# Performance work log

Measured on AMD Instinct MI355X. Metric: run time of the kernel, lower is better.

## Reference

```python
import jax, jax.numpy as jnp
import numpy as np

NUM_USERS = 10000
NUM_POIS = 50000
SEQ_LEN = 100
EMB = 128
HEADS = 8
NUM_NODES = NUM_USERS + NUM_POIS + 1  # +1 padding node (last row)
N_LOCAL = 2
N_GLOBAL = 2
B = 1024
NNZ_G = 1920000
NNZ_H = 1600000


def spmm(rows, cols, vals, x, n):
    # torch.sparse.mm(COO, x): gather rows of x by cols, scale, scatter-add by rows
    return jax.ops.segment_sum(vals[:, None] * x[cols], rows, num_segments=n)


def mha(x, in_w, in_b, out_w, out_b):
    # torch.nn.MultiheadAttention (batch_first, eval mode, self-attention)
    b, l, d = x.shape
    hd = d // HEADS
    qkv = x @ in_w.T + in_b  # [b, l, 3d]
    q, k, v = jnp.split(qkv, 3, axis=-1)
    def split_heads(t):
        return t.reshape(b, l, HEADS, hd).transpose(0, 2, 1, 3)  # [b,h,l,hd]
    q, k, v = split_heads(q), split_heads(k), split_heads(v)
    scores = jnp.einsum('bhqd,bhkd->bhqk', q, k) / jnp.sqrt(jnp.asarray(hd, x.dtype))
    attn = jax.nn.softmax(scores, axis=-1)
    o = jnp.einsum('bhqk,bhkd->bhqd', attn, v)
    o = o.transpose(0, 2, 1, 3).reshape(b, l, d)
    return o @ out_w.T + out_b


def setup_inputs():
    key = jax.random.key(0)
    ks = jax.random.split(key, 32)
    stdv = 1.0 / np.sqrt(EMB)
    def u(k, shape):
        return jax.random.uniform(k, shape, jnp.float32, -stdv, stdv)
    inp = {}
    # --- learned parameters ---
    inp['nodes_emb'] = u(ks[0], (NUM_NODES, EMB)).at[NUM_NODES - 1].set(0.0)  # padding_idx
    inp['pos_emb_local'] = u(ks[1], (SEQ_LEN + 1, EMB)).at[0].set(0.0)
    inp['fc_geo_w'] = u(ks[2], (EMB, EMB))
    inp['fc_geo_b'] = u(ks[3], (EMB,))
    inp['in_proj_w'] = u(ks[4], (3 * EMB, EMB))
    inp['in_proj_b'] = u(ks[5], (3 * EMB,))
    inp['out_proj_w'] = u(ks[6], (EMB, EMB))
    inp['out_proj_b'] = u(ks[7], (EMB,))
    inp['pos_emb_glob'] = u(ks[8], (SEQ_LEN + 1, EMB)).at[0].set(0.0)
    inp['w1_w'] = u(ks[9], (EMB, 2 * EMB))
    inp['w1_b'] = u(ks[10], (EMB,))
    inp['w_2'] = u(ks[11], (EMB, 1))
    inp['glu1_w'] = u(ks[12], (EMB, EMB))
    inp['glu1_b'] = u(ks[13], (EMB,))
    inp['glu2_w'] = u(ks[14], (EMB, EMB))
    # --- sparse graphs (COO) ---
    inp['G_rows'] = jax.random.randint(ks[15], (NNZ_G,), 0, NUM_NODES - 1, jnp.int32)
    inp['G_cols'] = jax.random.randint(ks[16], (NNZ_G,), 0, NUM_NODES - 1, jnp.int32)
    inp['G_vals'] = jax.random.uniform(ks[17], (NNZ_G,), jnp.float32) * (1.0 / 32.0)
    inp['HG_rows'] = jax.random.randint(ks[18], (NNZ_H,), 0, NUM_POIS, jnp.int32)
    inp['HG_cols'] = jax.random.randint(ks[19], (NNZ_H,), 0, NUM_POIS, jnp.int32)
    inp['HG_vals'] = jax.random.uniform(ks[20], (NNZ_H,), jnp.float32) * (1.0 / 32.0)
    # --- batch tensors ---
    inp['batch_users_seqs'] = jax.random.randint(ks[21], (B, SEQ_LEN), 0, NUM_NODES - 1, jnp.int32)
    inp['batch_users_seqs_masks'] = jax.random.randint(ks[22], (B, SEQ_LEN), 0, 2, jnp.int32)
    inp['batch_users_geo_adjs'] = jax.random.uniform(ks[23], (B, SEQ_LEN, SEQ_LEN), jnp.float32) * (1.0 / SEQ_LEN)
    inp['batch_users_indices'] = jnp.arange(B, dtype=jnp.int32)
    inp['batch_seqs_lens'] = 1.0 + jax.random.uniform(ks[24], (B,), jnp.float32) * (SEQ_LEN - 1)
    inp['batch_users_rev_seqs'] = jax.random.randint(ks[25], (B, SEQ_LEN), 0, NUM_NODES - 1, jnp.int32)
    return inp


def reference(nodes_emb, pos_emb_local, fc_geo_w, fc_geo_b, in_proj_w, in_proj_b,
              out_proj_w, out_proj_b, pos_emb_glob, w1_w, w1_b, w_2, glu1_w, glu1_b,
              glu2_w, G_rows, G_cols, G_vals, HG_rows, HG_cols, HG_vals,
              batch_users_seqs, batch_users_seqs_masks, batch_users_geo_adjs,
              batch_users_indices, batch_seqs_lens, batch_users_rev_seqs):
    pos_local = pos_emb_local[jnp.arange(1, SEQ_LEN + 1)]  # [L, D], same for all batches

    def st_layer(nodes):
        seq_e = nodes[batch_users_seqs]  # [B, L, D] gather
        geo_e = jnp.einsum('bls,bsd->bld', batch_users_geo_adjs, seq_e)
        geo_e = jax.nn.relu(geo_e @ fc_geo_w.T + fc_geo_b)
        tot = seq_e + pos_local[None] + geo_e
        o = mha(tot, in_proj_w, in_proj_b, out_proj_w, out_proj_b)
        users = jnp.mean(o, axis=1)  # [B, D]
        nodes = nodes.at[batch_users_indices].set(users)  # scatter
        core = spmm(G_rows, G_cols, G_vals, nodes[:-1], NUM_NODES - 1)
        return nodes.at[:-1].set(core)

    # local spatial-temporal graph: shared layer applied N_LOCAL times, layer-mean
    nodes = nodes_emb
    acc = nodes
    for _ in range(N_LOCAL):
        nodes = st_layer(nodes)
        acc = acc + nodes
    local = acc / (N_LOCAL + 1)

    local_users = local[batch_users_indices]
    local_pois = local[NUM_USERS:-1]

    # global hypergraph convolution on POI embeddings, layer-mean
    x = nodes_emb[NUM_USERS:-1]
    acc_g = x
    for _ in range(N_GLOBAL):
        x = spmm(HG_rows, HG_cols, HG_vals, x, NUM_POIS)
        acc_g = acc_g + x
    global_pois = acc_g / (N_GLOBAL + 1)

    pois_embs = local_pois + global_pois
    fusion = jnp.concatenate([local[:NUM_USERS], pois_embs,
                              jnp.zeros((1, EMB), local.dtype)], axis=0)

    # user temporal preference augmentation
    seq_h = fusion[batch_users_rev_seqs]  # [B, L, D]
    hs = jnp.sum(seq_h, axis=1) / batch_seqs_lens[:, None]  # [B, D]
    pos_idx = jnp.arange(1, SEQ_LEN + 1, dtype=jnp.int32)[None] * batch_users_seqs_masks
    pos_e = pos_emb_glob[pos_idx]  # [B, L, D]; masked positions hit padding row 0
    nh = jnp.tanh(jnp.concatenate([pos_e, seq_h], axis=-1) @ w1_w.T + w1_b)
    nh = jax.nn.sigmoid(nh @ glu1_w.T + glu1_b + hs[:, None, :] @ glu2_w.T)
    beta = nh @ w_2  # [B, L, 1]
    select = jnp.sum(beta * seq_h, axis=1)  # [B, D]

    batch_users_embs = select + local_users
    return batch_users_embs, pois_embs
```

## Files before the change

### kernel.cpp

```cpp
#include <hip/hip_runtime.h>
#include <hip/hip_bf16.h>
#include <math.h>

typedef __hip_bfloat16 bf16;

__device__ __forceinline__ float b2f(bf16 x){ return __bfloat162float(x); }
__device__ __forceinline__ bf16  f2b(float x){ return __float2bfloat16(x); }

__device__ __forceinline__ short f2bs(float f){
    unsigned u = __float_as_uint(f);
    u += 0x7fffu + ((u >> 16) & 1u);
    return (short)(u >> 16);
}
__device__ __forceinline__ float bs2f(short s){
    return __uint_as_float(((unsigned)(unsigned short)s) << 16);
}

#define NUSERS   10000
#define NPOIS    50000
#define SEQL     100
#define NNODES   60001
#define BATCH    1024
#define NNZG     1920000
#define NNZH     1600000
#define BL       (BATCH*SEQL)
#define BLD      (BL*128)
#define NND      (NNODES*128)
#define CN       (60000*128)
#define PD       (NPOIS*128)

__device__ __forceinline__ void  stc(bf16* p,  float v){ *p = f2b(v); }
__device__ __forceinline__ void  stc(float* p, float v){ *p = v; }

typedef __attribute__((ext_vector_type(8))) short s16x8;
typedef __attribute__((ext_vector_type(4))) float f32x4;

__global__ __launch_bounds__(256) void k_zero(float* __restrict__ p, int n4){
    int i = blockIdx.x*256 + threadIdx.x;
    if (i < n4) ((float4*)p)[i] = make_float4(0.f,0.f,0.f,0.f);
}

__global__ __launch_bounds__(256) void k_copy16(ulong2* __restrict__ dst,
                                                const ulong2* __restrict__ src, int n16){
    int i = blockIdx.x*256 + threadIdx.x;
    if (i < n16) dst[i] = src[i];
}

__global__ __launch_bounds__(256) void k_init(bf16* __restrict__ nodes, float* __restrict__ acc,
                                              const float* __restrict__ src, int n){
    int i = blockIdx.x*256 + threadIdx.x;
    if (i >= n) return;
    float v = src[i];
    nodes[i] = f2b(v); acc[i] = v;
}

__global__ __launch_bounds__(256) void k_gather_f(float* __restrict__ dst,
                                                  const float* __restrict__ table,
                                                  const int* __restrict__ idx, int rows){
    int gid = blockIdx.x*256 + threadIdx.x;
    if (gid >= rows*128) return;
    int r = gid >> 7, c = gid & 127;
    dst[(size_t)r*128 + c] = table[(size_t)idx[r]*128 + c];
}

__global__ __launch_bounds__(256) void k_mgeo2(bf16* __restrict__ tot,
                                               const bf16* __restrict__ nodes,
                                               const int* __restrict__ seqs,
                                               const float* __restrict__ adj,
                                               const float* __restrict__ fcw,
                                               const float* __restrict__ fcb,
                                               const float* __restrict__ posl){
    __shared__ short st[128*104];
    __shared__ short gt[112*136];
    int b = blockIdx.x, tid = threadIdx.x;
    const int* sq = seqs + b*SEQL;
    for (int i = tid; i < SEQL*128; i += 256){
        int j = i >> 7, c = i & 127;
        st[c*104 + j] = ((const short*)nodes)[(size_t)sq[j]*128 + c];
    }
    for (int i = tid; i < 128*4; i += 256){ int c = i>>2, r = i&3; st[c*104 + 100 + r] = 0; }
    __syncthreads();
    int wv = tid>>6, lane = tid&63, lr = lane&15, lk = lane>>4;
    const s16x8 zf = {0,0,0,0,0,0,0,0};
    s16x8 bfr[2][4];
    #pragma unroll
    for (int t = 0; t < 2; t++){
        int nt = wv*2 + t;
        #pragma unroll
        for (int kc = 0; kc < 4; kc++)
            bfr[t][kc] = *(const s16x8*)&st[(nt*16+lr)*104 + kc*32 + lk*8];
    }
    const float* ab = adj + (size_t)b*SEQL*SEQL;
    for (int mt = 0; mt < 7; mt++){
        int ar = min(mt*16 + lr, SEQL-1);
        s16x8 ah[4], al[4];
        #pragma unroll
        for (int kc = 0; kc < 4; kc++){
            float av[8] = {0,0,0,0,0,0,0,0};
            if (kc < 3){
                const float* ap = ab + (size_t)ar*SEQL + kc*32 + lk*8;
                float4 a0 = *(const float4*)ap;
                float4 a1 = *(const float4*)(ap + 4);
                av[0]=a0.x; av[1]=a0.y; av[2]=a0.z; av[3]=a0.w;
                av[4]=a1.x; av[5]=a1.y; av[6]=a1.z; av[7]=a1.w;
            } else if (lk == 0){
                float4 a0 = *(const float4*)(ab + (size_t)ar*SEQL + 96);
                av[0]=a0.x; av[1]=a0.y; av[2]=a0.z; av[3]=a0.w;
            }
            s16x8 h = zf, l = zf;
            #pragma unroll
            for (int j = 0; j < 8; j++){
                short hb = f2bs(av[j]);
                h[j] = hb;
                l[j] = f2bs(av[j] - bs2f(hb));
            }
            ah[kc] = h; al[kc] = l;
        }
        f32x4 c0 = {0.f,0.f,0.f,0.f}, c1 = {0.f,0.f,0.f,0.f};
        #pragma unroll
        for (int kc = 0; kc < 4; kc++){
            c0 = __builtin_amdgcn_mfma_f32_16x16x32_bf16(ah[kc], bfr[0][kc], c0, 0,0,0);
            c0 = __builtin_amdgcn_mfma_f32_16x16x32_bf16(al[kc], bfr[0][kc], c0, 0,0,0);
            c1 = __builtin_amdgcn_mfma_f32_16x16x32_bf16(ah[kc], bfr[1][kc], c1, 0,0,0);
            c1 = __builtin_amdgcn_mfma_f32_16x16x32_bf16(al[kc], bfr[1][kc], c1, 0,0,0);
        }
        #pragma unroll
        for (int t = 0; t < 2; t++){
            f32x4 cc = t ? c1 : c0;
            int col = wv*32 + t*16 + lr;
            #pragma unroll
            for (int r = 0; r < 4; r++){
                int row = mt*16 + lk*4 + r;
                gt[row*136 + col] = f2bs(cc[r]);
            }
        }
    }
    s16x8 wh[2][4], wl[2][4];
    int n0 = wv*32;
    #pragma unroll
    for (int t = 0; t < 2; t++){
        #pragma unroll
        for (int ks = 0; ks < 4; ks++){
            const float* wp = fcw + (size_t)(n0 + t*16 + lr)*128 + ks*32 + lk*8;
            float4 w0 = *(const float4*)(wp);
            float4 w1 = *(const float4*)(wp + 4);
            float wf[8] = {w0.x,w0.y,w0.z,w0.w,w1.x,w1.y,w1.z,w1.w};
            s16x8 h, l;
            #pragma unroll
            for (int j = 0; j < 8; j++){
                short hb = f2bs(wf[j]);
                h[j] = hb;
                l[j] = f2bs(wf[j] - bs2f(hb));
            }
            wh[t][ks] = h; wl[t][ks] = l;
        }
    }
    __syncthreads();
    for (int mt = 0; mt < 7; mt++){
        s16x8 ah[4];
        #pragma unroll
        for (int ks = 0; ks < 4; ks++)
            ah[ks] = *(const s16x8*)&gt[(mt*16+lr)*136 + ks*32 + lk*8];
        f32x4 c0 = {0.f,0.f,0.f,0.f}, c1 = {0.f,0.f,0.f,0.f};
        #pragma unroll
        for (int ks = 0; ks < 4; ks++){
            c0 = __builtin_amdgcn_mfma_f32_16x16x32_bf16(ah[ks], wh[0][ks], c0, 0,0,0);
            c0 = __builtin_amdgcn_mfma_f32_16x16x32_bf16(ah[ks], wl[0][ks], c0, 0,0,0);
            c1 = __builtin_amdgcn_mfma_f32_16x16x32_bf16(ah[ks], wh[1][ks], c1, 0,0,0);
            c1 = __builtin_amdgcn_mfma_f32_16x16x32_bf16(ah[ks], wl[1][ks], c1, 0,0,0);
        }
        #pragma unroll
        for (int t = 0; t < 2; t++){
            f32x4 cc = t ? c1 : c0;
            int col = n0 + t*16 + lr;
            float bv = fcb[col];
            #pragma unroll
            for (int r = 0; r < 4; r++){
                int row = mt*16 + lk*4 + r;
                if (row < SEQL){
                    float v = fmaxf(cc[r] + bv, 0.f);
                    v += bs2f(st[col*104 + row]) + posl[(row+1)*128 + col];
                    tot[(size_t)b*SEQL*128 + (size_t)row*128 + col] = f2b(v);
                }
            }
        }
    }
}

template<typename TA, typename TC>
__global__ __launch_bounds__(256) void k_mgemm(const TA* __restrict__ A,
                                               const float* __restrict__ W, int wstride, int woff,
                                               const float* __restrict__ bias, int boff,
                                               TC* __restrict__ C, int act,
                                               const float* __restrict__ add1, int addmode,
                                               const int* __restrict__ masks){
    constexpr bool A_BF = (sizeof(TA) == 2);
    int tid  = threadIdx.x;
    int wv   = tid >> 6;
    int lane = tid & 63;
    int lr   = lane & 15;
    int lk   = lane >> 4;
    int n0   = wv * 32;

    s16x8 wh[2][4], wl[2][4];
    #pragma unroll
    for (int t = 0; t < 2; t++){
        #pragma unroll
        for (int ks = 0; ks < 4; ks++){
            const float* wp = W + (size_t)(n0 + t*16 + lr)*wstride + woff + ks*32 + lk*8;
            float4 w0 = *(const float4*)(wp);
            float4 w1 = *(const float4*)(wp + 4);
            float wf[8] = {w0.x,w0.y,w0.z,w0.w,w1.x,w1.y,w1.z,w1.w};
            s16x8 h, l;
            #pragma unroll
            for (int j = 0; j < 8; j++){
                short hb = f2bs(wf[j]);
                h[j] = hb;
                l[j] = f2bs(wf[j] - bs2f(hb));
            }
            wh[t][ks] = h; wl[t][ks] = l;
        }
    }

    size_t mblk = (size_t)blockIdx.x * 128;
    for (int it = 0; it < 8; it++){
        size_t m0 = mblk + (size_t)it*16;
        s16x8 ah[4], al[4];
        #pragma unroll
        for (int ks = 0; ks < 4; ks++){
            if constexpr (A_BF){
                ah[ks] = *(const s16x8*)((const short*)A + (m0 + lr)*128 + ks*32 + lk*8);
            } else {
                const float* ap = (const float*)A + (m0 + lr)*128 + ks*32 + lk*8;
                float4 a0 = *(const float4*)(ap);
                float4 a1 = *(const float4*)(ap + 4);
                float av[8] = {a0.x,a0.y,a0.z,a0.w,a1.x,a1.y,a1.z,a1.w};
                s16x8 h, l;
                #pragma unroll
                for (int j = 0; j < 8; j++){
                    short hb = f2bs(av[j]);
                    h[j] = hb;
                    l[j] = f2bs(av[j] - bs2f(hb));
                }
                ah[ks] = h; al[ks] = l;
            }
        }
        __syncthreads();
        f32x4 c0 = {0.f,0.f,0.f,0.f}, c1 = {0.f,0.f,0.f,0.f};
        #pragma unroll
        for (int ks = 0; ks < 4; ks++){
            c0 = __builtin_amdgcn_mfma_f32_16x16x32_bf16(ah[ks], wh[0][ks], c0, 0, 0, 0);
            c0 = __builtin_amdgcn_mfma_f32_16x16x32_bf16(ah[ks], wl[0][ks], c0, 0, 0, 0);
            c1 = __builtin_amdgcn_mfma_f32_16x16x32_bf16(ah[ks], wh[1][ks], c1, 0, 0, 0);
            c1 = __builtin_amdgcn_mfma_f32_16x16x32_bf16(ah[ks], wl[1][ks], c1, 0, 0, 0);
            if constexpr (!A_BF){
                c0 = __builtin_amdgcn_mfma_f32_16x16x32_bf16(al[ks], wh[0][ks], c0, 0, 0, 0);
                c1 = __builtin_amdgcn_mfma_f32_16x16x32_bf16(al[ks], wh[1][ks], c1, 0, 0, 0);
            }
        }
        #pragma unroll
        for (int t = 0; t < 2; t++){
            f32x4 cc = t ? c1 : c0;
            int c = n0 + t*16 + lr;
            float bv = bias ? bias[boff + c] : 0.f;
            #pragma unroll
            for (int r4 = 0; r4 < 4; r4++){
                int m = (int)m0 + lk*4 + r4;
                float v = cc[r4] + bv;
                if (addmode == 1){
                    int l = m % SEQL;
                    int p = (l+1) * masks[m];
                    v += add1[p*128 + c];
                } else if (addmode == 2){
                    v += add1[(m/SEQL)*128 + c];
                }
                if (act == 1) v = fmaxf(v, 0.f);
                else if (act == 2) v = tanhf(v);
                else if (act == 3) v = 1.f/(1.f+__expf(-v));
                stc(&C[(size_t)m*128 + c], v);
            }
        }
    }
}

__global__ __launch_bounds__(256) void k_mattn(bf16* o, const bf16* Qq,
                                               const bf16* Qk, const bf16* Qv){
    __shared__ short Vt[128*104];
    __shared__ short Ph[4][16*136];
    __shared__ short Pl[4][16*136];
    int b = blockIdx.x, tid = threadIdx.x;
    const short* vsrc = (const short*)(Qv + (size_t)b*SEQL*128);
    for (int i = tid; i < SEQL*128; i += 256){ int j = i>>7, c = i&127; Vt[c*104 + j] = vsrc[i]; }
    for (int i = tid; i < 128*4; i += 256){ int c = i>>2, r = i&3; Vt[c*104 + 100 + r] = 0; }
    int wv = tid>>6, lane = tid&63, lr = lane&15, lk = lane>>4;
    short* phw = Ph[wv];
    short* plw = Pl[wv];
    for (int i = lane; i < 16*136; i += 64){ phw[i] = 0; plw[i] = 0; }
    __syncthreads();

    const s16x8 zf = {0,0,0,0,0,0,0,0};
    size_t rowbase = (size_t)b*SEQL*128;
    bool kreal = (lk < 2);
    for (int hh = 0; hh < 2; hh++){
        int h = wv*2 + hh;
        int hd = h*16 + lk*8;
        s16x8 kf[7];
        #pragma unroll
        for (int nt = 0; nt < 7; nt++){
            int kr = min(nt*16 + lr, SEQL-1);
            kf[nt] = kreal ? *(const s16x8*)((const short*)Qk + rowbase + (size_t)kr*128 + hd) : zf;
        }
        s16x8 vf[4];
        #pragma unroll
        for (int kc = 0; kc < 4; kc++)
            vf[kc] = *(const s16x8*)&Vt[(h*16+lr)*104 + kc*32 + lk*8];

        for (int mt = 0; mt < 7; mt++){
            int qr = min(mt*16 + lr, SEQL-1);
            s16x8 qf = kreal ? *(const s16x8*)((const short*)Qq + rowbase + (size_t)qr*128 + hd) : zf;
            f32x4 sc[7];
            #pragma unroll
            for (int nt = 0; nt < 7; nt++){
                f32x4 z = {0.f,0.f,0.f,0.f};
                sc[nt] = __builtin_amdgcn_mfma_f32_16x16x32_bf16(qf, kf[nt], z, 0,0,0);
            }
            float mx[4] = {-1e30f,-1e30f,-1e30f,-1e30f};
            #pragma unroll
            for (int nt = 0; nt < 7; nt++){
                bool masked = (nt == 6) && (lr >= 4);
                #pragma unroll
                for (int r = 0; r < 4; r++){
                    float s = masked ? -1e30f : sc[nt][r]*0.25f;
                    sc[nt][r] = s;
                    mx[r] = fmaxf(mx[r], s);
                }
            }
            #pragma unroll
            for (int m = 1; m < 16; m <<= 1){
                #pragma unroll
                for (int r = 0; r < 4; r++) mx[r] = fmaxf(mx[r], __shfl_xor(mx[r], m));
            }
            float sm[4] = {0.f,0.f,0.f,0.f};
            #pragma unroll
            for (int nt = 0; nt < 7; nt++){
                #pragma unroll
                for (int r = 0; r < 4; r++){
                    float p = __expf(sc[nt][r] - mx[r]);
                    sc[nt][r] = p; sm[r] += p;
                }
            }
            #pragma unroll
            for (int m = 1; m < 16; m <<= 1){
                #pragma unroll
                for (int r = 0; r < 4; r++) sm[r] += __shfl_xor(sm[r], m);
            }
            float inv[4];
            #pragma unroll
            for (int r = 0; r < 4; r++) inv[r] = 1.f/sm[r];
            #pragma unroll
            for (int nt = 0; nt < 7; nt++){
                #pragma unroll
                for (int r = 0; r < 4; r++){
                    float p = sc[nt][r]*inv[r];
                    short hb = f2bs(p);
                    int pa = (lk*4+r)*136 + nt*16 + lr;
                    phw[pa] = hb;
                    plw[pa] = f2bs(p - bs2f(hb));
                }
            }
            f32x4 oa = {0.f,0.f,0.f,0.f};
            #pragma unroll
            for (int kc = 0; kc < 4; kc++){
                s16x8 pah = *(const s16x8*)&phw[lr*136 + kc*32 + lk*8];
                s16x8 pal = *(const s16x8*)&plw[lr*136 + kc*32 + lk*8];
                oa = __builtin_amdgcn_mfma_f32_16x16x32_bf16(pah, vf[kc], oa, 0,0,0);
                oa = __builtin_amdgcn_mfma_f32_16x16x32_bf16(pal, vf[kc], oa, 0,0,0);
            }
            #pragma unroll
            for (int r = 0; r < 4; r++){
                int row = mt*16 + lk*4 + r;
                if (row < SEQL)
                    ((short*)o)[rowbase + (size_t)row*128 + h*16 + lr] = f2bs(oa[r]);
            }
        }
    }
}

__global__ __launch_bounds__(128) void k_mean_users(bf16* __restrict__ nodes,
                                                    const bf16* __restrict__ o,
                                                    const int* __restrict__ uidx){
    int b = blockIdx.x, c = threadIdx.x;
    const bf16* p = o + (size_t)b*SEQL*128 + c;
    float sum = 0.f;
    for (int l = 0; l < SEQL; l++) sum += b2f(p[l*128]);
    nodes[(size_t)uidx[b]*128 + c] = f2b(sum * (1.f/(float)SEQL));
}


__global__ __launch_bounds__(256) void k_hist(int* __restrict__ cnt,
                                              const int* __restrict__ rows, int nnz){
    int e = blockIdx.x*256 + threadIdx.x;
    if (e < nnz) atomicAdd(&cnt[rows[e]], 1);
}

__global__ __launch_bounds__(1024) void k_scan(int* __restrict__ cnt,
                                               int* __restrict__ rowptr, int nrows){
    __shared__ int part[1024];
    int tid = threadIdx.x;
    int chunk = (nrows + 1023) >> 10;
    int s = tid*chunk, e = min(s+chunk, nrows);
    int sum = 0;
    for (int i = s; i < e; i++) sum += cnt[i];
    part[tid] = sum;
    __syncthreads();
    for (int off = 1; off < 1024; off <<= 1){
        int add = (tid >= off) ? part[tid-off] : 0;
        __syncthreads();
        part[tid] += add;
        __syncthreads();
    }
    int run = part[tid] - sum;
    for (int i = s; i < e; i++){
        int c = cnt[i];
        rowptr[i] = run;
        cnt[i]    = run;
        run += c;
    }
    if (tid == 0) rowptr[nrows] = part[1023];
}

__global__ __launch_bounds__(256) void k_scatter(int2* __restrict__ cv,
                                                 int* __restrict__ cur,
                                                 const int* __restrict__ rows,
                                                 const int* __restrict__ cols,
                                                 const float* __restrict__ vals, int nnz){
    int e = blockIdx.x*256 + threadIdx.x;
    if (e >= nnz) return;
    int p = atomicAdd(&cur[rows[e]], 1);
    cv[p] = make_int2(cols[e], __float_as_int(vals[e]));
}

__global__ __launch_bounds__(256) void k_spmm_csr(bf16* __restrict__ yb,
                                                  float* __restrict__ acc,
                                                  const int* __restrict__ rowptr,
                                                  const int2* __restrict__ cv,
                                                  const bf16* __restrict__ x, int nrows){
    int row = blockIdx.x*4 + (threadIdx.x >> 6);
    if (row >= nrows) return;
    int lane = threadIdx.x & 63;
    int g = lane >> 4;
    int t = lane & 15;
    int s = rowptr[row], e = rowptr[row+1];
    float a[8] = {0.f,0.f,0.f,0.f,0.f,0.f,0.f,0.f};
    for (int i = s + g; i < e; i += 4){
        int2 p = cv[i];
        float v = __int_as_float(p.y);
        uint4 u = *(const uint4*)(x + (size_t)p.x*128 + t*8);
        unsigned w0 = u.x, w1 = u.y, w2 = u.z, w3 = u.w;
        a[0] += v * __uint_as_float((w0 & 0xffffu) << 16);
        a[1] += v * __uint_as_float(w0 & 0xffff0000u);
        a[2] += v * __uint_as_float((w1 & 0xffffu) << 16);
        a[3] += v * __uint_as_float(w1 & 0xffff0000u);
        a[4] += v * __uint_as_float((w2 & 0xffffu) << 16);
        a[5] += v * __uint_as_float(w2 & 0xffff0000u);
        a[6] += v * __uint_as_float((w3 & 0xffffu) << 16);
        a[7] += v * __uint_as_float(w3 & 0xffff0000u);
    }
    #pragma unroll
    for (int j = 0; j < 8; j++){
        a[j] += __shfl_xor(a[j], 16);
        a[j] += __shfl_xor(a[j], 32);
    }
    if (g == 0){
        s16x8 ob;
        #pragma unroll
        for (int j = 0; j < 8; j++) ob[j] = f2bs(a[j]);
        *(s16x8*)((short*)yb + (size_t)row*128 + t*8) = ob;
        float* ap = acc + (size_t)row*128 + t*8;
        float4 c0 = ((float4*)ap)[0], c1 = ((float4*)ap)[1];
        c0.x += a[0]; c0.y += a[1]; c0.z += a[2]; c0.w += a[3];
        c1.x += a[4]; c1.y += a[5]; c1.z += a[6]; c1.w += a[7];
        ((float4*)ap)[0] = c0; ((float4*)ap)[1] = c1;
    }
}

__global__ __launch_bounds__(256) void k_scale(float* __restrict__ a, int n){
    int i = blockIdx.x*256 + threadIdx.x;
    if (i < n) a[i] *= (1.f/3.f);
}

__global__ __launch_bounds__(256) void k_initg(bf16* __restrict__ xg, float* __restrict__ accg,
                                               const float* __restrict__ ne, int n){
    int i = blockIdx.x*256 + threadIdx.x;
    if (i >= n) return;
    float v = ne[(size_t)NUSERS*128 + i];
    xg[i] = f2b(v); accg[i] = v;
}

__global__ __launch_bounds__(256) void k_fusion(float* __restrict__ accP,
                                                const float* __restrict__ accg,
                                                float* __restrict__ outp, int n){
    int i = blockIdx.x*256 + threadIdx.x;
    if (i >= n) return;
    float v = accP[i] + accg[i]*(1.f/3.f);
    accP[i] = v;
    outp[i] = v;
}


__global__ __launch_bounds__(128) void k_hs(float* __restrict__ hs, const float* __restrict__ sh,
                                            const float* __restrict__ lens){
    int b = blockIdx.x, c = threadIdx.x;
    const float* p = sh + (size_t)b*SEQL*128 + c;
    float sum = 0.f;
    for (int l = 0; l < SEQL; l++) sum += p[l*128];
    hs[b*128 + c] = sum / lens[b];
}

__global__ __launch_bounds__(128) void k_posw(float* __restrict__ posW,
                                              const float* __restrict__ pg,
                                              const float* __restrict__ w1w){
    __shared__ float sm[128];
    int p = blockIdx.x, n = threadIdx.x;
    sm[n] = pg[p*128 + n];
    __syncthreads();
    const float* wr = w1w + (size_t)n*256;
    float s = 0.f;
    for (int k = 0; k < 128; k++) s += sm[k]*wr[k];
    posW[p*128 + n] = s;
}

__global__ __launch_bounds__(256) void k_beta(float* __restrict__ beta,
                                              const bf16* __restrict__ nh,
                                              const float* __restrict__ w2){
    int m = blockIdx.x*4 + (threadIdx.x >> 6);
    int lane = threadIdx.x & 63;
    float v = b2f(nh[(size_t)m*128 + lane]) * w2[lane]
            + b2f(nh[(size_t)m*128 + 64 + lane]) * w2[64 + lane];
    #pragma unroll
    for (int s = 1; s < 64; s <<= 1) v += __shfl_xor(v, s);
    if (lane == 0) beta[m] = v;
}

__global__ __launch_bounds__(128) void k_final(float* __restrict__ out,
                                               const float* __restrict__ beta,
                                               const float* __restrict__ seqh,
                                               const float* __restrict__ acc,
                                               const int* __restrict__ uidx){
    int b = blockIdx.x, c = threadIdx.x;
    const float* sh = seqh + (size_t)b*SEQL*128 + c;
    const float* bp = beta + b*SEQL;
    float sel = 0.f;
    for (int l = 0; l < SEQL; l++) sel += bp[l]*sh[l*128];
    out[b*128 + c] = sel + acc[(size_t)uidx[b]*128 + c];
}

extern "C" void kernel_launch(void* const* d_in, const int* in_sizes, int n_in,
                              void* d_out, int out_size, void* d_ws, size_t ws_size,
                              hipStream_t stream){
    const float* nodes_emb     = (const float*)d_in[0];
    const float* pos_emb_local = (const float*)d_in[1];
    const float* fc_geo_w      = (const float*)d_in[2];
    const float* fc_geo_b      = (const float*)d_in[3];
    const float* in_proj_w     = (const float*)d_in[4];
    const float* in_proj_b     = (const float*)d_in[5];
    const float* out_proj_w    = (const float*)d_in[6];
    const float* out_proj_b    = (const float*)d_in[7];
    const float* pos_emb_glob  = (const float*)d_in[8];
    const float* w1_w          = (const float*)d_in[9];
    const float* w1_b          = (const float*)d_in[10];
    const float* w_2           = (const float*)d_in[11];
    const float* glu1_w        = (const float*)d_in[12];
    const float* glu1_b        = (const float*)d_in[13];
    const float* glu2_w        = (const float*)d_in[14];
    const int*   G_rows        = (const int*)d_in[15];
    const int*   G_cols        = (const int*)d_in[16];
    const float* G_vals        = (const float*)d_in[17];
    const int*   HG_rows       = (const int*)d_in[18];
    const int*   HG_cols       = (const int*)d_in[19];
    const float* HG_vals       = (const float*)d_in[20];
    const int*   seqs          = (const int*)d_in[21];
    const int*   masks         = (const int*)d_in[22];
    const float* adjs          = (const float*)d_in[23];
    const int*   uidx          = (const int*)d_in[24];
    const float* lens          = (const float*)d_in[25];
    const int*   rev_seqs      = (const int*)d_in[26];
    float* out = (float*)d_out;

    char* base = (char*)d_ws;
    bf16*  nodes = (bf16*)base;
    float* acc   = (float*)(base + 15360256);
    char*  R     = base + 15360256 + 30720512;
    bf16* P1 = (bf16*)R;
    bf16* P2 = P1 + BLD;
    bf16* P3 = P2 + BLD;
    bf16*  xsnap = (bf16*)R;
    int2*  Gcv  = (int2*)(R + 30720000);
    int*   Gptr = (int*)(R + 46080000);
    int*   Gcur = (int*)(R + 46320016);
    bf16*  xg     = (bf16*)R;
    bf16*  xsnapg = (bf16*)(R + 12800000);
    float* accg = (float*)(R + 12800000 + 25600000);
    int2*  Hcv  = (int2*)(R + 64000000);
    int*   Hptr = (int*)(R + 76800000);
    int*   Hcur = (int*)(R + 77000016);
    float* H1f  = (float*)R;
    bf16*  nh   = (bf16*)(R + 52428800);
    float* hs    = (float*)base;
    float* hproj = (float*)(base + 524288);
    float* posW  = (float*)(base + 1048576);
    float* betaB = (float*)(base + 1100288);

    auto gemm = [&](const bf16* A, const float* W, int wstride, int woff,
                    const float* bias, int boff, bf16* Cp, int act){
        k_mgemm<bf16,bf16><<<dim3(BL/128), dim3(256), 0, stream>>>(
            A, W, wstride, woff, bias, boff, Cp, act, nullptr, 0, nullptr);
    };

    k_init<<<dim3((NND+255)/256), dim3(256), 0, stream>>>(nodes, acc, nodes_emb, NND);

    for (int layer = 0; layer < 2; layer++){
        k_mgeo2<<<dim3(BATCH), dim3(256), 0, stream>>>(P3, nodes, seqs, adjs,
                                                       fc_geo_w, fc_geo_b, pos_emb_local);
        gemm(P3, in_proj_w, 128, 0,       in_proj_b, 0,   P1, 0);
        gemm(P3, in_proj_w, 128, 128*128, in_proj_b, 128, P2, 0);
        gemm(P3, in_proj_w, 128, 256*128, in_proj_b, 256, P3, 0);
        k_mattn<<<dim3(BATCH), dim3(256), 0, stream>>>(P1, P1, P2, P3);
        gemm(P1, out_proj_w, 128, 0, out_proj_b, 0, P2, 0);
        k_mean_users<<<dim3(BATCH), dim3(128), 0, stream>>>(nodes, P2, uidx);
        k_zero<<<dim3((15000+255)/256), dim3(256), 0, stream>>>((float*)Gcur, 15000);
        k_hist<<<dim3(NNZG/256), dim3(256), 0, stream>>>(Gcur, G_rows, NNZG);
        k_scan<<<dim3(1), dim3(1024), 0, stream>>>(Gcur, Gptr, 60000);
        k_scatter<<<dim3(NNZG/256), dim3(256), 0, stream>>>(Gcv, Gcur, G_rows, G_cols, G_vals, NNZG);
        k_copy16<<<dim3((960000+255)/256), dim3(256), 0, stream>>>(
            (ulong2*)xsnap, (const ulong2*)nodes, 960000);
        k_spmm_csr<<<dim3(60000/4), dim3(256), 0, stream>>>(nodes, acc, Gptr, Gcv, xsnap, 60000);
    }
    k_scale<<<dim3((NND+255)/256), dim3(256), 0, stream>>>(acc, NND);

    k_initg<<<dim3((PD+255)/256), dim3(256), 0, stream>>>(xg, accg, nodes_emb, PD);
    k_zero<<<dim3((12500+255)/256), dim3(256), 0, stream>>>((float*)Hcur, 12500);
    k_hist<<<dim3(NNZH/256), dim3(256), 0, stream>>>(Hcur, HG_rows, NNZH);
    k_scan<<<dim3(1), dim3(1024), 0, stream>>>(Hcur, Hptr, 50000);
    k_scatter<<<dim3(NNZH/256), dim3(256), 0, stream>>>(Hcv, Hcur, HG_rows, HG_cols, HG_vals, NNZH);
    for (int it = 0; it < 2; it++){
        k_copy16<<<dim3((800000+255)/256), dim3(256), 0, stream>>>(
            (ulong2*)xsnapg, (const ulong2*)xg, 800000);
        k_spmm_csr<<<dim3(50000/4), dim3(256), 0, stream>>>(xg, accg, Hptr, Hcv, xsnapg, 50000);
    }
    k_fusion<<<dim3((PD+255)/256), dim3(256), 0, stream>>>(acc + (size_t)NUSERS*128, accg, out + BATCH*128, PD);

    k_gather_f<<<dim3((BL*128+255)/256), dim3(256), 0, stream>>>(H1f, acc, rev_seqs, BL);
    k_hs<<<dim3(BATCH), dim3(128), 0, stream>>>(hs, H1f, lens);
    k_mgemm<float,float><<<dim3(BATCH/128), dim3(256), 0, stream>>>(
        hs, glu2_w, 128, 0, nullptr, 0, hproj, 0, nullptr, 0, nullptr);
    k_posw<<<dim3(SEQL+1), dim3(128), 0, stream>>>(posW, pos_emb_glob, w1_w);
    k_mgemm<float,bf16><<<dim3(BL/128), dim3(256), 0, stream>>>(
        H1f, w1_w, 256, 128, w1_b, 0, nh, 2, posW, 1, masks);
    k_mgemm<bf16,bf16><<<dim3(BL/128), dim3(256), 0, stream>>>(
        nh, glu1_w, 128, 0, glu1_b, 0, nh, 3, hproj, 2, nullptr);
    k_beta<<<dim3(BL/4), dim3(256), 0, stream>>>(betaB, nh, w_2);
    k_final<<<dim3(BATCH), dim3(128), 0, stream>>>(out, betaB, H1f, acc, uidx);
}
```

Baseline: 2.329 ms.

## Fuse sequence mean into attention, hoist CSR build out of layer loop, widen SpMM lanes

The attention kernel now averages its output over the sequence in registers, and the output projection is applied only to the 1024 per-user means instead of all B*L rows. This relies on the projection being linear, and it drops one full-size GEMM and the separate mean kernel. The graph CSR build (hist, scan, scatter) moves out of the layer loop so it runs once, with its buffers placed in the output buffer's scratch region. The SpMM kernel is changed to use 8 edge groups per row with 16 columns per lane.

After: 1.968 ms. 1.18x faster.

```diff
diff --git a/kernel.cpp b/kernel.cpp
--- a/kernel.cpp
+++ b/kernel.cpp
@@ -193,7 +193,8 @@
                                                const float* __restrict__ bias, int boff,
                                                TC* __restrict__ C, int act,
                                                const float* __restrict__ add1, int addmode,
-                                               const int* __restrict__ masks){
+                                               const int* __restrict__ masks,
+                                               const int* __restrict__ outidx){
     constexpr bool A_BF = (sizeof(TA) == 2);
     int tid  = threadIdx.x;
     int wv   = tid >> 6;
@@ -277,14 +278,17 @@
                 if (act == 1) v = fmaxf(v, 0.f);
                 else if (act == 2) v = tanhf(v);
                 else if (act == 3) v = 1.f/(1.f+__expf(-v));
-                stc(&C[(size_t)m*128 + c], v);
-            }
-        }
-    }
-}
-
-__global__ __launch_bounds__(256) void k_mattn(bf16* o, const bf16* Qq,
-                                               const bf16* Qk, const bf16* Qv){
+                size_t orow = outidx ? (size_t)outidx[m] : (size_t)m;
+                stc(&C[orow*128 + c], v);
+            }
+        }
+    }
+}
+
+__global__ __launch_bounds__(256) void k_mattn(float* __restrict__ Omean,
+                                               const bf16* __restrict__ Qq,
+                                               const bf16* __restrict__ Qk,
+                                               const bf16* __restrict__ Qv){
     __shared__ short Vt[128*104];
     __shared__ short Ph[4][16*136];
     __shared__ short Pl[4][16*136];
@@ -315,6 +319,7 @@
         for (int kc = 0; kc < 4; kc++)
             vf[kc] = *(const s16x8*)&Vt[(h*16+lr)*104 + kc*32 + lk*8];
 
+        float msum = 0.f;
         for (int mt = 0; mt < 7; mt++){
             int qr = min(mt*16 + lr, SEQL-1);
             s16x8 qf = kreal ? *(const s16x8*)((const short*)Qq + rowbase + (size_t)qr*128 + hd) : zf;
@@ -379,21 +384,13 @@
             #pragma unroll
             for (int r = 0; r < 4; r++){
                 int row = mt*16 + lk*4 + r;
-                if (row < SEQL)
-                    ((short*)o)[rowbase + (size_t)row*128 + h*16 + lr] = f2bs(oa[r]);
-            }
-        }
-    }
-}
-
-__global__ __launch_bounds__(128) void k_mean_users(bf16* __restrict__ nodes,
-                                                    const bf16* __restrict__ o,
-                                                    const int* __restrict__ uidx){
-    int b = blockIdx.x, c = threadIdx.x;
-    const bf16* p = o + (size_t)b*SEQL*128 + c;
-    float sum = 0.f;
-    for (int l = 0; l < SEQL; l++) sum += b2f(p[l*128]);
-    nodes[(size_t)uidx[b]*128 + c] = f2b(sum * (1.f/(float)SEQL));
+                if (row < SEQL) msum += oa[r];
+            }
+        }
+        msum += __shfl_xor(msum, 16);
+        msum += __shfl_xor(msum, 32);
+        if (lk == 0) Omean[(size_t)b*128 + h*16 + lr] = msum * (1.f/(float)SEQL);
+    }
 }
 
 
@@ -448,39 +445,45 @@
     int row = blockIdx.x*4 + (threadIdx.x >> 6);
     if (row >= nrows) return;
     int lane = threadIdx.x & 63;
-    int g = lane >> 4;
-    int t = lane & 15;
+    int g = lane >> 3;
+    int t = lane & 7;
     int s = rowptr[row], e = rowptr[row+1];
-    float a[8] = {0.f,0.f,0.f,0.f,0.f,0.f,0.f,0.f};
-    for (int i = s + g; i < e; i += 4){
+    float a[16];
+    #pragma unroll
+    for (int j = 0; j < 16; j++) a[j] = 0.f;
+    for (int i = s + g; i < e; i += 8){
         int2 p = cv[i];
         float v = __int_as_float(p.y);
-        uint4 u = *(const uint4*)(x + (size_t)p.x*128 + t*8);
-        unsigned w0 = u.x, w1 = u.y, w2 = u.z, w3 = u.w;
-        a[0] += v * __uint_as_float((w0 & 0xffffu) << 16);
-        a[1] += v * __uint_as_float(w0 & 0xffff0000u);
-        a[2] += v * __uint_as_float((w1 & 0xffffu) << 16);
-        a[3] += v * __uint_as_float(w1 & 0xffff0000u);
-        a[4] += v * __uint_as_float((w2 & 0xffffu) << 16);
-        a[5] += v * __uint_as_float(w2 & 0xffff0000u);
-        a[6] += v * __uint_as_float((w3 & 0xffffu) << 16);
-        a[7] += v * __uint_as_float(w3 & 0xffff0000u);
+        const unsigned* xp = (const unsigned*)(x + (size_t)p.x*128 + t*16);
+        uint4 u0 = *(const uint4*)xp;
+        uint4 u1 = *(const uint4*)(xp + 4);
+        unsigned w[8] = {u0.x,u0.y,u0.z,u0.w,u1.x,u1.y,u1.z,u1.w};
+        #pragma unroll
+        for (int j = 0; j < 8; j++){
+            a[2*j]   += v * __uint_as_float((w[j] & 0xffffu) << 16);
+            a[2*j+1] += v * __uint_as_float(w[j] & 0xffff0000u);
+        }
     }
     #pragma unroll
-    for (int j = 0; j < 8; j++){
+    for (int j = 0; j < 16; j++){
+        a[j] += __shfl_xor(a[j], 8);
         a[j] += __shfl_xor(a[j], 16);
         a[j] += __shfl_xor(a[j], 32);
     }
     if (g == 0){
-        s16x8 ob;
-        #pragma unroll
-        for (int j = 0; j < 8; j++) ob[j] = f2bs(a[j]);
-        *(s16x8*)((short*)yb + (size_t)row*128 + t*8) = ob;
-        float* ap = acc + (size_t)row*128 + t*8;
-        float4 c0 = ((float4*)ap)[0], c1 = ((float4*)ap)[1];
-        c0.x += a[0]; c0.y += a[1]; c0.z += a[2]; c0.w += a[3];
-        c1.x += a[4]; c1.y += a[5]; c1.z += a[6]; c1.w += a[7];
-        ((float4*)ap)[0] = c0; ((float4*)ap)[1] = c1;
+        s16x8 o0, o1;
+        #pragma unroll
+        for (int j = 0; j < 8; j++){ o0[j] = f2bs(a[j]); o1[j] = f2bs(a[8+j]); }
+        short* yp = (short*)yb + (size_t)row*128 + t*16;
+        *(s16x8*)yp = o0;
+        *(s16x8*)(yp + 8) = o1;
+        float* ap = acc + (size_t)row*128 + t*16;
+        #pragma unroll
+        for (int q = 0; q < 4; q++){
+            float4 c = ((float4*)ap)[q];
+            c.x += a[q*4+0]; c.y += a[q*4+1]; c.z += a[q*4+2]; c.w += a[q*4+3];
+            ((float4*)ap)[q] = c;
+        }
     }
 }
 
@@ -595,9 +598,6 @@
     bf16* P2 = P1 + BLD;
     bf16* P3 = P2 + BLD;
     bf16*  xsnap = (bf16*)R;
-    int2*  Gcv  = (int2*)(R + 30720000);
-    int*   Gptr = (int*)(R + 46080000);
-    int*   Gcur = (int*)(R + 46320016);
     bf16*  xg     = (bf16*)R;
     bf16*  xsnapg = (bf16*)(R + 12800000);
     float* accg = (float*)(R + 12800000 + 25600000);
@@ -610,14 +610,24 @@
     float* hproj = (float*)(base + 524288);
     float* posW  = (float*)(base + 1048576);
     float* betaB = (float*)(base + 1100288);
+    char*  ob    = (char*)out;
+    int2*  Gcv   = (int2*)ob;
+    int*   Gptr  = (int*)(ob + 15360000);
+    int*   Gcur  = (int*)(ob + 15600016);
+    float* Omean = (float*)(ob + 15840016);
 
     auto gemm = [&](const bf16* A, const float* W, int wstride, int woff,
                     const float* bias, int boff, bf16* Cp, int act){
         k_mgemm<bf16,bf16><<<dim3(BL/128), dim3(256), 0, stream>>>(
-            A, W, wstride, woff, bias, boff, Cp, act, nullptr, 0, nullptr);
+            A, W, wstride, woff, bias, boff, Cp, act, nullptr, 0, nullptr, nullptr);
     };
 
     k_init<<<dim3((NND+255)/256), dim3(256), 0, stream>>>(nodes, acc, nodes_emb, NND);
+
+    k_zero<<<dim3((15000+255)/256), dim3(256), 0, stream>>>((float*)Gcur, 15000);
+    k_hist<<<dim3(NNZG/256), dim3(256), 0, stream>>>(Gcur, G_rows, NNZG);
+    k_scan<<<dim3(1), dim3(1024), 0, stream>>>(Gcur, Gptr, 60000);
+    k_scatter<<<dim3(NNZG/256), dim3(256), 0, stream>>>(Gcv, Gcur, G_rows, G_cols, G_vals, NNZG);
 
     for (int layer = 0; layer < 2; layer++){
         k_mgeo2<<<dim3(BATCH), dim3(256), 0, stream>>>(P3, nodes, seqs, adjs,
@@ -625,13 +635,9 @@
         gemm(P3, in_proj_w, 128, 0,       in_proj_b, 0,   P1, 0);
         gemm(P3, in_proj_w, 128, 128*128, in_proj_b, 128, P2, 0);
         gemm(P3, in_proj_w, 128, 256*128, in_proj_b, 256, P3, 0);
-        k_mattn<<<dim3(BATCH), dim3(256), 0, stream>>>(P1, P1, P2, P3);
-        gemm(P1, out_proj_w, 128, 0, out_proj_b, 0, P2, 0);
-        k_mean_users<<<dim3(BATCH), dim3(128), 0, stream>>>(nodes, P2, uidx);
-        k_zero<<<dim3((15000+255)/256), dim3(256), 0, stream>>>((float*)Gcur, 15000);
-        k_hist<<<dim3(NNZG/256), dim3(256), 0, stream>>>(Gcur, G_rows, NNZG);
-        k_scan<<<dim3(1), dim3(1024), 0, stream>>>(Gcur, Gptr, 60000);
-        k_scatter<<<dim3(NNZG/256), dim3(256), 0, stream>>>(Gcv, Gcur, G_rows, G_cols, G_vals, NNZG);
+        k_mattn<<<dim3(BATCH), dim3(256), 0, stream>>>(Omean, P1, P2, P3);
+        k_mgemm<float,bf16><<<dim3(BATCH/128), dim3(256), 0, stream>>>(
+            Omean, out_proj_w, 128, 0, out_proj_b, 0, nodes, 0, nullptr, 0, nullptr, uidx);
         k_copy16<<<dim3((960000+255)/256), dim3(256), 0, stream>>>(
             (ulong2*)xsnap, (const ulong2*)nodes, 960000);
         k_spmm_csr<<<dim3(60000/4), dim3(256), 0, stream>>>(nodes, acc, Gptr, Gcv, xsnap, 60000);
@@ -653,12 +659,12 @@
     k_gather_f<<<dim3((BL*128+255)/256), dim3(256), 0, stream>>>(H1f, acc, rev_seqs, BL);
     k_hs<<<dim3(BATCH), dim3(128), 0, stream>>>(hs, H1f, lens);
     k_mgemm<float,float><<<dim3(BATCH/128), dim3(256), 0, stream>>>(
-        hs, glu2_w, 128, 0, nullptr, 0, hproj, 0, nullptr, 0, nullptr);
+        hs, glu2_w, 128, 0, nullptr, 0, hproj, 0, nullptr, 0, nullptr, nullptr);
     k_posw<<<dim3(SEQL+1), dim3(128), 0, stream>>>(posW, pos_emb_glob, w1_w);
     k_mgemm<float,bf16><<<dim3(BL/128), dim3(256), 0, stream>>>(
-        H1f, w1_w, 256, 128, w1_b, 0, nh, 2, posW, 1, masks);
+        H1f, w1_w, 256, 128, w1_b, 0, nh, 2, posW, 1, masks, nullptr);
     k_mgemm<bf16,bf16><<<dim3(BL/128), dim3(256), 0, stream>>>(
-        nh, glu1_w, 128, 0, glu1_b, 0, nh, 3, hproj, 2, nullptr);
+        nh, glu1_w, 128, 0, glu1_b, 0, nh, 3, hproj, 2, nullptr, nullptr);
     k_beta<<<dim3(BL/4), dim3(256), 0, stream>>>(betaB, nh, w_2);
     k_final<<<dim3(BATCH), dim3(128), 0, stream>>>(out, betaB, H1f, acc, uidx);
 }
```
